# Kernel optimization log

Hardware: AMD Instinct MI355X
Metric: run time of the kernel (lower is better)

The kernel has to match this reference:

```python
import jax, jax.numpy as jnp
import numpy as np

B, S, D, H = 1, 2048, 4096, 32
HD = D // H
THETA = 10000.0
IN_SCALE = 0.1   # input_scale buffer
Q_SCALE = 0.1    # q_proj_scale buffer
K_SCALE = 0.1    # k_proj_scale buffer
V_SCALE = 0.1    # v_proj_scale buffer
OUT_SCALE = 0.1  # out_input_scale buffer


def _fake_q(x, scale, lo, hi):
    # round-to-int + clamp, kept in float (faithful to int8 fake-quant)
    return jnp.clip(jnp.round(x / scale), lo, hi)


def _w4a8_linear(x, qw, w_scale, in_scale):
    # int8 fake-quantized activation x int4-valued weight, dequant output
    qx = _fake_q(x, in_scale, -128, 127)
    return jnp.einsum('bsd,od->bso', qx, qw) * (in_scale * w_scale)


def _rope_tables(position_ids):
    inv_freq = 1.0 / (THETA ** (jnp.arange(0, HD, 2, dtype=jnp.float32) / HD))
    ang = position_ids.astype(jnp.float32)[..., None] * inv_freq  # [B,S,HD/2]
    emb = jnp.concatenate([ang, ang], axis=-1)                     # [B,S,HD]
    return jnp.cos(emb)[:, None], jnp.sin(emb)[:, None]            # [B,1,S,HD]


def _rotate_half(x):
    return jnp.concatenate([-x[..., HD // 2:], x[..., :HD // 2]], axis=-1)


def setup_inputs() -> dict:
    key = jax.random.key(0)
    ks = jax.random.split(key, 9)
    hidden_states = jax.random.normal(ks[0], (B, S, D), jnp.float32)
    def int4_w(k):
        return jnp.round(jax.random.uniform(k, (D, D), jnp.float32, -8.0, 7.0))
    def ch_scale(k):
        return jax.random.uniform(k, (D,), jnp.float32, 0.01, 0.03)
    wq, wk, wv, wo = int4_w(ks[1]), int4_w(ks[2]), int4_w(ks[3]), int4_w(ks[4])
    sq_w, sk_w, sv_w, so_w = ch_scale(ks[5]), ch_scale(ks[6]), ch_scale(ks[7]), ch_scale(ks[8])
    position_ids = jnp.arange(S, dtype=jnp.int32)[None, :]
    causal = jnp.tril(jnp.ones((S, S), dtype=bool))
    attention_mask = jnp.where(causal, 0.0, -1e9).astype(jnp.float32)[None, None]
    return dict(hidden_states=hidden_states, wq=wq, wk=wk, wv=wv, wo=wo,
                sq_w=sq_w, sk_w=sk_w, sv_w=sv_w, so_w=so_w,
                attention_mask=attention_mask, position_ids=position_ids)


def reference(hidden_states, wq, wk, wv, wo, sq_w, sk_w, sv_w, so_w,
              attention_mask, position_ids):
    # W4A8 dequant projections
    q = _w4a8_linear(hidden_states, wq, sq_w, IN_SCALE)
    k = _w4a8_linear(hidden_states, wk, sk_w, IN_SCALE)
    v = _w4a8_linear(hidden_states, wv, sv_w, IN_SCALE)
    q = q.reshape(B, S, H, HD).transpose(0, 2, 1, 3)  # [B,H,S,HD]
    k = k.reshape(B, S, H, HD).transpose(0, 2, 1, 3)
    v = v.reshape(B, S, H, HD).transpose(0, 2, 1, 3)
    # RoPE
    cos, sin = _rope_tables(position_ids)
    q = q * cos + _rotate_half(q) * sin
    k = k * cos + _rotate_half(k) * sin
    # int8 fake-quant of q/k/v, then dequant before matmuls
    q = _fake_q(q, Q_SCALE, -128, 127)
    k = _fake_q(k, K_SCALE, -128, 127)
    v = _fake_q(v, V_SCALE, -128, 127)
    scores = jnp.einsum('bhqd,bhkd->bhqk', q * Q_SCALE, k * K_SCALE) / np.sqrt(HD)
    scores = scores + attention_mask
    attn = jax.nn.softmax(scores.astype(jnp.float32), axis=-1)
    out = jnp.einsum('bhqk,bhkd->bhqd', attn, v * V_SCALE)
    out = out.transpose(0, 2, 1, 3).reshape(B, S, D)
    # o_proj input re-quantized to int8 with out_input_scale (clamp -127..127)
    out_q = _fake_q(out, OUT_SCALE, -127, 127)
    attn_output = jnp.einsum('bsd,od->bso', out_q, wo) * (OUT_SCALE * so_w)
    return attn_output
```

## Files before the change

kernel.cpp:

```cpp
#include <hip/hip_runtime.h>
#include <math.h>
#include <stdint.h>

#define S_LEN 2048
#define D_DIM 4096
#define NHEAD 32
#define HDIM  128

typedef int      v4i __attribute__((ext_vector_type(4)));
typedef float    v4f __attribute__((ext_vector_type(4)));
typedef _Float16 v8h __attribute__((ext_vector_type(8)));

__device__ __forceinline__ float quant128(float x) {
  return fminf(fmaxf(rintf(x / 0.1f), -128.f), 127.f);
}
__device__ __forceinline__ void gl_lds16(const void* g, void* l) {
  __builtin_amdgcn_global_load_lds(
      (const __attribute__((address_space(1))) void*)g,
      (__attribute__((address_space(3))) void*)l, 16, 0, 0);
}

__global__ __launch_bounds__(256) void quant_hidden_k(const float* __restrict__ in,
                                                      int8_t* __restrict__ out) {
  const int idx = blockIdx.x * 256 + threadIdx.x;
  const float4 v = ((const float4*)in)[idx];
  const int q0 = (int)quant128(v.x), q1 = (int)quant128(v.y);
  const int q2 = (int)quant128(v.z), q3 = (int)quant128(v.w);
  ((int*)out)[idx] = (q0 & 0xff) | ((q1 & 0xff) << 8) | ((q2 & 0xff) << 16) | ((q3 & 0xff) << 24);
}

__global__ __launch_bounds__(256) void wconv3_k(const float* __restrict__ a,
                                                const float* __restrict__ b,
                                                const float* __restrict__ c,
                                                int8_t* __restrict__ out) {
  const int which = blockIdx.x >> 14;
  const int sub = blockIdx.x & 16383;
  const float* src = (which == 0) ? a : (which == 1) ? b : c;
  const int idx = sub * 256 + threadIdx.x;
  const float4 v = ((const float4*)src)[idx];
  const int q0 = __float2int_rn(v.x), q1 = __float2int_rn(v.y);
  const int q2 = __float2int_rn(v.z), q3 = __float2int_rn(v.w);
  ((int*)out)[(size_t)which * 4194304 + idx] =
      (q0 & 0xff) | ((q1 & 0xff) << 8) | ((q2 & 0xff) << 16) | ((q3 & 0xff) << 24);
}

__global__ __launch_bounds__(256) void wconv_k(const float* __restrict__ in,
                                               int8_t* __restrict__ out) {
  const int idx = blockIdx.x * 256 + threadIdx.x;
  const float4 v = ((const float4*)in)[idx];
  const int q0 = __float2int_rn(v.x), q1 = __float2int_rn(v.y);
  const int q2 = __float2int_rn(v.z), q3 = __float2int_rn(v.w);
  ((int*)out)[idx] = (q0 & 0xff) | ((q1 & 0xff) << 8) | ((q2 & 0xff) << 16) | ((q3 & 0xff) << 24);
}

__global__ __launch_bounds__(256) void rope_tab_k(const int* __restrict__ pos,
                                                  float* __restrict__ ct,
                                                  float* __restrict__ st) {
  const int idx = blockIdx.x * 256 + threadIdx.x;
  const int s = idx >> 6, j = idx & 63;
  const float inv = exp2f((float)j * -0.20762050593046016f);
  const float a = (float)pos[s] * inv;
  float si, c;
  sincosf(a, &si, &c);
  ct[idx] = c;
  st[idx] = si;
}

template <int MODE>
__device__ __forceinline__ void gemm_body(
    int8_t* __restrict__ LS, const int8_t* __restrict__ A8,
    const int8_t* __restrict__ W8, const float* __restrict__ s0,
    const float* __restrict__ s1, const float* __restrict__ s2,
    const float* __restrict__ ctab, const float* __restrict__ stab,
    void* __restrict__ out0, void* __restrict__ out1, void* __restrict__ out2,
    int nwg) {
  int8_t* const Abase = LS;
  int8_t* const Bbase = LS + 49152;

  const int t = threadIdx.x;
  const int w = t >> 6, lane = t & 63, g = lane >> 4, l15 = lane & 15;
  const int wm = w >> 2, wn = w & 3;

  const int bid = blockIdx.x;
  const int lb = (bid & 7) * (nwg >> 3) + (bid >> 3);
  const int within = lb & 15, g16 = lb >> 4;
  const int bm = ((g16 & 1) * 4 + (within >> 2)) * 256;
  const int bn = ((g16 >> 1) * 4 + (within & 3)) * 256;

  const int8_t* srcA[2];
  const int8_t* srcB[2];
  int sdst[2];
#pragma unroll
  for (int i = 0; i < 2; ++i) {
    const int lin = i * 512 + t;
    const int row = lin >> 2;
    const int sc = (lin & 3) ^ ((row >> 1) & 3);
    srcA[i] = A8 + (size_t)(bm + row) * D_DIM + sc * 16;
    srcB[i] = W8 + (size_t)(bn + row) * D_DIM + sc * 16;
    sdst[i] = lin * 16;
  }

#define STAGE(KT, BI)                                                       \
  {                                                                         \
    const int kof_ = (KT) * 64;                                             \
    _Pragma("unroll") for (int i_ = 0; i_ < 2; ++i_) {                      \
      gl_lds16(srcA[i_] + kof_, Abase + (BI) * 16384 + sdst[i_]);           \
      gl_lds16(srcB[i_] + kof_, Bbase + (BI) * 16384 + sdst[i_]);           \
    }                                                                       \
  }

  const int cg = ((g ^ ((l15 >> 1) & 3)) << 4);
  const int nc0 = (wn & 1) * 32 + (wn >> 1) * 128;
  int aoffs[8], boffs[4];
#pragma unroll
  for (int mi = 0; mi < 8; ++mi)
    aoffs[mi] = (wm * 128 + mi * 16 + l15) * 64 + cg;
#pragma unroll
  for (int ni = 0; ni < 4; ++ni)
    boffs[ni] = (nc0 + (ni & 1) * 16 + (ni >> 1) * 64 + l15) * 64 + cg;

  v4i acc[8][4];
#pragma unroll
  for (int mi = 0; mi < 8; ++mi)
#pragma unroll
    for (int ni = 0; ni < 4; ++ni) acc[mi][ni] = (v4i){0, 0, 0, 0};

  STAGE(0, 0)
  STAGE(1, 1)
  asm volatile("s_waitcnt vmcnt(4)" ::: "memory");
  __builtin_amdgcn_s_barrier();
  __builtin_amdgcn_sched_barrier(0);

  for (int t3 = 0; t3 < 66; t3 += 3) {
#pragma unroll
    for (int u = 0; u < 3; ++u) {
      const int kt = t3 + u;
      if (kt < 64) {
        if (kt + 2 < 64) STAGE(kt + 2, ((u + 2) % 3))
        v4i af[8], bf[4];
        {
          const int8_t* Ab_ = Abase + u * 16384;
          const int8_t* Bb_ = Bbase + u * 16384;
#pragma unroll
          for (int mi = 0; mi < 8; ++mi) af[mi] = *(const v4i*)(Ab_ + aoffs[mi]);
#pragma unroll
          for (int ni = 0; ni < 4; ++ni) bf[ni] = *(const v4i*)(Bb_ + boffs[ni]);
        }
        __builtin_amdgcn_s_setprio(1);
#pragma unroll
        for (int mi = 0; mi < 8; ++mi)
#pragma unroll
          for (int ni = 0; ni < 4; ++ni)
            acc[mi][ni] = __builtin_amdgcn_mfma_i32_16x16x64_i8(
                af[mi], bf[ni], acc[mi][ni], 0, 0, 0);
        __builtin_amdgcn_s_setprio(0);
        if (kt + 2 < 64)
          asm volatile("s_waitcnt vmcnt(4)" ::: "memory");
        else
          asm volatile("s_waitcnt vmcnt(0)" ::: "memory");
        __builtin_amdgcn_s_barrier();
        __builtin_amdgcn_sched_barrier(0);
      }
    }
  }
#undef STAGE

  const int srow0 = bm + wm * 128;
  if (MODE == 1) {
    float* dst = (float*)out0;
#pragma unroll
    for (int ni = 0; ni < 4; ++ni) {
      const int col = bn + nc0 + (ni & 1) * 16 + (ni >> 1) * 64 + l15;
      const float sc = 0.1f * s0[col];
#pragma unroll
      for (int mi = 0; mi < 8; ++mi)
#pragma unroll
        for (int r = 0; r < 4; ++r)
          dst[(size_t)(srow0 + mi * 16 + g * 4 + r) * D_DIM + col] =
              (float)acc[mi][ni][r] * sc;
    }
  } else {
    const int seg = bn >> 12;
    const int bcol = bn & 4095;
    if (seg == 2) {
      _Float16* dst = (_Float16*)out2;
#pragma unroll
      for (int ni = 0; ni < 4; ++ni) {
        const int col = bcol + nc0 + (ni & 1) * 16 + (ni >> 1) * 64 + l15;
        const float scv = 0.1f * s2[col];
#pragma unroll
        for (int mi = 0; mi < 8; ++mi)
#pragma unroll
          for (int r = 0; r < 4; ++r) {
            const int s = srow0 + mi * 16 + g * 4 + r;
            dst[(size_t)col * S_LEN + s] = (_Float16)quant128((float)acc[mi][ni][r] * scv);
          }
      }
    } else {
      const float* wsc = seg ? s1 : s0;
      int8_t* dst = seg ? (int8_t*)out1 : (int8_t*)out0;
      const int hb = bcol + (wn >> 1) * 128;
#pragma unroll
      for (int ni = 0; ni < 2; ++ni) {
        const int dlo = (wn & 1) * 32 + ni * 16 + l15;
        const int clo = hb + dlo;
        const float sc0 = 0.1f * wsc[clo];
        const float sc1 = 0.1f * wsc[clo + 64];
#pragma unroll
        for (int mi = 0; mi < 8; ++mi)
#pragma unroll
          for (int r = 0; r < 4; ++r) {
            const int s = srow0 + mi * 16 + g * 4 + r;
            const float c = ctab[s * 64 + dlo];
            const float si = stab[s * 64 + dlo];
            const float x1 = (float)acc[mi][ni][r] * sc0;
            const float x2 = (float)acc[mi][ni + 2][r] * sc1;
            dst[(size_t)s * D_DIM + clo] = (int8_t)quant128(x1 * c - x2 * si);
            dst[(size_t)s * D_DIM + clo + 64] = (int8_t)quant128(x2 * c + x1 * si);
          }
      }
    }
  }
}

__global__ __launch_bounds__(512) void gemm_qkv(
    const int8_t* __restrict__ A8, const int8_t* __restrict__ W8,
    const float* __restrict__ s0, const float* __restrict__ s1,
    const float* __restrict__ s2, const float* __restrict__ ctab,
    const float* __restrict__ stab, void* __restrict__ out0,
    void* __restrict__ out1, void* __restrict__ out2) {
  __shared__ __align__(16) int8_t LS[6 * 16384];
  gemm_body<0>(LS, A8, W8, s0, s1, s2, ctab, stab, out0, out1, out2, 384);
}

__global__ __launch_bounds__(512) void gemm_out(
    const int8_t* __restrict__ A8, const int8_t* __restrict__ W8,
    const float* __restrict__ s0, const float* __restrict__ ctab,
    const float* __restrict__ stab, void* __restrict__ out0) {
  __shared__ __align__(16) int8_t LS[6 * 16384];
  gemm_body<1>(LS, A8, W8, s0, s0, s0, ctab, stab, out0, out0, out0, 128);
}

__global__ __launch_bounds__(512, 4) void attn_v8(
    const int8_t* __restrict__ q8, const int8_t* __restrict__ k8,
    const _Float16* __restrict__ vT, int8_t* __restrict__ o8) {
  __shared__ __align__(16) int8_t Kls[3][8192];
  __shared__ __align__(16) int8_t Vls[3][16384];
  const int jj = 15 - blockIdx.x;
  const int h = blockIdx.y;
  const int t = threadIdx.x;
  const int w = t >> 6, lane = t & 63, g = lane >> 4, l15 = lane & 15;
  const int T = 2 * jj + 2;
  const int q0 = (jj * 8 + w) * 16;
  const int q_lane = q0 + l15;
  const float SSCALE = 8.838834764831845e-4f;
  const v8h vones = {(_Float16)1, (_Float16)1, (_Float16)1, (_Float16)1,
                     (_Float16)1, (_Float16)1, (_Float16)1, (_Float16)1};

  const int ks_slot = t >> 3;
  const int ks_cs = (t & 7) ^ (ks_slot & 7);
  const int ks_key = ((ks_slot >> 5) & 1) * 32 + ((ks_slot >> 3) & 1) * 16 +
                     ((ks_slot >> 2) & 1) * 8 + ((ks_slot >> 4) & 1) * 4 +
                     (ks_slot & 3);
  const int k_src = ks_key * D_DIM + ks_cs * 16;
  const int k_dst = t * 16;
  int v_src[2], v_dst[2];
#pragma unroll
  for (int i = 0; i < 2; ++i) {
    const int lin = i * 512 + t;
    const int d = lin >> 3;
    const int cs = (lin & 7) ^ (d & 7);
    v_src[i] = d * S_LEN + cs * 8;
    v_dst[i] = lin * 16;
  }
  const int8_t* kbg = k8 + (size_t)h * HDIM;
  const _Float16* vbg = vT + (size_t)h * HDIM * S_LEN;

  auto stage = [&](int kt, int b) {
    const int8_t* ks = kbg + (size_t)kt * (64 * D_DIM);
    const _Float16* vs = vbg + kt * 64;
    gl_lds16(ks + k_src, &Kls[b][k_dst]);
#pragma unroll
    for (int i = 0; i < 2; ++i) gl_lds16(vs + v_src[i], &Vls[b][v_dst[i]]);
  };

  const v4i qa0 = *(const v4i*)(q8 + (size_t)q_lane * D_DIM + h * HDIM + g * 16);
  const v4i qa1 = *(const v4i*)(q8 + (size_t)q_lane * D_DIM + h * HDIM + 64 + g * 16);

  v4f o[8];
#pragma unroll
  for (int n = 0; n < 8; ++n) o[n] = (v4f){0.f, 0.f, 0.f, 0.f};
  v4f lacc = (v4f){0.f, 0.f, 0.f, 0.f};
  float m_i = -INFINITY;

  stage(0, 0);
  if (T > 1) stage(1, 1);

  int bi = 0;
  for (int kt = 0; kt < T; ++kt) {
    if (kt + 1 < T)
      asm volatile("s_waitcnt vmcnt(3)" ::: "memory");
    else
      asm volatile("s_waitcnt vmcnt(0)" ::: "memory");
    __builtin_amdgcn_s_barrier();
    __builtin_amdgcn_sched_barrier(0);
    if (kt + 2 < T) stage(kt + 2, bi >= 1 ? bi - 1 : bi + 2);

    const int ksw = (l15 & 7);
    float sc[4][4];
#pragma unroll
    for (int nt = 0; nt < 4; ++nt) {
      const int8_t* kr = &Kls[bi][(nt * 16 + l15) * 128];
      const v4i kb0 = *(const v4i*)(kr + ((g ^ ksw) * 16));
      const v4i kb1 = *(const v4i*)(kr + (((4 + g) ^ ksw) * 16));
      v4i c = (v4i){0, 0, 0, 0};
      c = __builtin_amdgcn_mfma_i32_16x16x64_i8(kb0, qa0, c, 0, 0, 0);
      c = __builtin_amdgcn_mfma_i32_16x16x64_i8(kb1, qa1, c, 0, 0, 0);
#pragma unroll
      for (int r = 0; r < 4; ++r) {
        float s = (float)c[r] * SSCALE;
        if (kt >= T - 2) {
          const int key = kt * 64 + ((nt >> 1) << 5) + ((g >> 1) << 4) +
                          ((g & 1) << 3) + ((nt & 1) << 2) + r;
          if (key > q_lane) s = -1.0e30f;
        }
        sc[nt][r] = s;
      }
    }
    float mx = fmaxf(fmaxf(fmaxf(sc[0][0], sc[0][1]), fmaxf(sc[0][2], sc[0][3])),
                     fmaxf(fmaxf(sc[1][0], sc[1][1]), fmaxf(sc[1][2], sc[1][3])));
    mx = fmaxf(mx, fmaxf(fmaxf(fmaxf(sc[2][0], sc[2][1]), fmaxf(sc[2][2], sc[2][3])),
                         fmaxf(fmaxf(sc[3][0], sc[3][1]), fmaxf(sc[3][2], sc[3][3]))));
    mx = fmaxf(mx, __shfl_xor(mx, 16));
    mx = fmaxf(mx, __shfl_xor(mx, 32));
    const float mnew = fmaxf(m_i, mx);
    const float alpha = __expf(m_i - mnew);
    m_i = mnew;

    float p[4][4];
#pragma unroll
    for (int nt = 0; nt < 4; ++nt)
#pragma unroll
      for (int r = 0; r < 4; ++r) p[nt][r] = __expf(sc[nt][r] - m_i);

    v8h ph0, ph1;
#pragma unroll
    for (int e = 0; e < 8; ++e) {
      ph0[e] = (_Float16)p[e >> 2][e & 3];
      ph1[e] = (_Float16)p[2 + (e >> 2)][e & 3];
    }
    float a_r[4];
#pragma unroll
    for (int r = 0; r < 4; ++r)
      a_r[r] = __shfl(alpha, (lane & 48) | (g * 4 + r));
#pragma unroll
    for (int n = 0; n < 8; ++n)
#pragma unroll
      for (int r = 0; r < 4; ++r) o[n][r] *= a_r[r];
#pragma unroll
    for (int r = 0; r < 4; ++r) lacc[r] *= a_r[r];

    __builtin_amdgcn_s_setprio(1);
    lacc = __builtin_amdgcn_mfma_f32_16x16x32_f16(ph0, vones, lacc, 0, 0, 0);
    lacc = __builtin_amdgcn_mfma_f32_16x16x32_f16(ph1, vones, lacc, 0, 0, 0);
#pragma unroll
    for (int nt = 0; nt < 8; ++nt) {
      const int8_t* vr = &Vls[bi][(nt * 16 + l15) * 128];
      const v8h v0 = *(const v8h*)(vr + ((g ^ ksw) * 16));
      const v8h v1 = *(const v8h*)(vr + (((4 + g) ^ ksw) * 16));
      o[nt] = __builtin_amdgcn_mfma_f32_16x16x32_f16(ph0, v0, o[nt], 0, 0, 0);
      o[nt] = __builtin_amdgcn_mfma_f32_16x16x32_f16(ph1, v1, o[nt], 0, 0, 0);
    }
    __builtin_amdgcn_s_setprio(0);

    bi = (bi == 2) ? 0 : bi + 1;
  }

#pragma unroll
  for (int r = 0; r < 4; ++r) {
    const float rL = 1.0f / lacc[r];
    const size_t row = (size_t)(q0 + g * 4 + r) * D_DIM + h * HDIM;
#pragma unroll
    for (int nt = 0; nt < 8; ++nt) {
      const int q = (int)fminf(fmaxf(rintf(o[nt][r] * rL), -127.f), 127.f);
      o8[row + nt * 16 + l15] = (int8_t)q;
    }
  }
}

extern "C" void kernel_launch(void* const* d_in, const int* in_sizes, int n_in,
                              void* d_out, int out_size, void* d_ws, size_t ws_size,
                              hipStream_t stream) {
  (void)in_sizes; (void)n_in; (void)out_size; (void)ws_size;
  const float* hidden = (const float*)d_in[0];
  const float* wq = (const float*)d_in[1];
  const float* wk = (const float*)d_in[2];
  const float* wv = (const float*)d_in[3];
  const float* wo = (const float*)d_in[4];
  const float* sq = (const float*)d_in[5];
  const float* sk = (const float*)d_in[6];
  const float* sv = (const float*)d_in[7];
  const float* so = (const float*)d_in[8];
  const int* pos = (const int*)d_in[10];
  float* out = (float*)d_out;

  char* ws = (char*)d_ws;
  int8_t* h8 = (int8_t*)ws;
  int8_t* q8 = (int8_t*)(ws + (8ull << 20));
  int8_t* k8 = (int8_t*)(ws + (16ull << 20));
  _Float16* vT = (_Float16*)(ws + (24ull << 20));
  int8_t* w8a = (int8_t*)(ws + (40ull << 20));
  int8_t* w8b = (int8_t*)(ws + (56ull << 20));
  int8_t* w8c = (int8_t*)(ws + (72ull << 20));
  float* ctab = (float*)(ws + (88ull << 20));
  float* stab = (float*)(ws + (88ull << 20) + (512ull << 10));
  int8_t* o8 = h8;

  hipLaunchKernelGGL(rope_tab_k, dim3(512), dim3(256), 0, stream, pos, ctab, stab);
  hipLaunchKernelGGL(quant_hidden_k, dim3(8192), dim3(256), 0, stream, hidden, h8);
  hipLaunchKernelGGL(wconv3_k, dim3(49152), dim3(256), 0, stream, wq, wk, wv, w8a);

  hipLaunchKernelGGL(gemm_qkv, dim3(384), dim3(512), 0, stream, h8, w8a,
                     sq, sk, sv, ctab, stab, (void*)q8, (void*)k8, (void*)vT);
  hipLaunchKernelGGL(wconv_k, dim3(16384), dim3(256), 0, stream, wo, w8a);
  hipLaunchKernelGGL(attn_v8, dim3(16, 32), dim3(512), 0, stream, q8, k8, vT, o8);
  hipLaunchKernelGGL(gemm_out, dim3(128), dim3(512), 0, stream, o8, w8a,
                     so, ctab, stab, (void*)out);
}
```

Before: 557.3 us.

## Halve GEMM M-tile to 128 and restructure pipeline with wait-before-stage loop

Shrinks the int8 GEMM block tile from 256x256 to 128x256, doubling the workgroup count for the QKV and output projections so more of the 256 CUs are occupied. Accumulators drop from 8x4 to 4x4 per wave, LDS shrinks to 72KB, and launch bounds ask for more resident blocks. The triple-buffer loop is rewritten to wait and barrier at the top of each iteration before issuing the next stage, instead of at the bottom. The cost is less reuse of each loaded B tile, which raises global and L2 traffic per MFMA.

```diff
diff --git a/kernel.cpp b/kernel.cpp
--- a/kernel.cpp
+++ b/kernel.cpp
@@ -75,7 +75,7 @@
     void* __restrict__ out0, void* __restrict__ out1, void* __restrict__ out2,
     int nwg) {
   int8_t* const Abase = LS;
-  int8_t* const Bbase = LS + 49152;
+  int8_t* const Bbase = LS + 24576;
 
   const int t = threadIdx.x;
   const int w = t >> 6, lane = t & 63, g = lane >> 4, l15 = lane & 15;
@@ -84,88 +84,84 @@
   const int bid = blockIdx.x;
   const int lb = (bid & 7) * (nwg >> 3) + (bid >> 3);
   const int within = lb & 15, g16 = lb >> 4;
-  const int bm = ((g16 & 1) * 4 + (within >> 2)) * 256;
-  const int bn = ((g16 >> 1) * 4 + (within & 3)) * 256;
-
-  const int8_t* srcA[2];
+  const int bm = ((g16 & 3) * 4 + (within >> 2)) * 128;
+  const int bn = ((g16 >> 2) * 4 + (within & 3)) * 256;
+
+  const int arow = t >> 2;
+  const int asc = (t & 3) ^ ((arow >> 1) & 3);
+  const int8_t* srcA = A8 + (size_t)(bm + arow) * D_DIM + asc * 16;
+  const int adst = t * 16;
   const int8_t* srcB[2];
-  int sdst[2];
+  int bdst[2];
 #pragma unroll
   for (int i = 0; i < 2; ++i) {
     const int lin = i * 512 + t;
     const int row = lin >> 2;
     const int sc = (lin & 3) ^ ((row >> 1) & 3);
-    srcA[i] = A8 + (size_t)(bm + row) * D_DIM + sc * 16;
     srcB[i] = W8 + (size_t)(bn + row) * D_DIM + sc * 16;
-    sdst[i] = lin * 16;
+    bdst[i] = lin * 16;
   }
 
 #define STAGE(KT, BI)                                                       \
   {                                                                         \
     const int kof_ = (KT) * 64;                                             \
-    _Pragma("unroll") for (int i_ = 0; i_ < 2; ++i_) {                      \
-      gl_lds16(srcA[i_] + kof_, Abase + (BI) * 16384 + sdst[i_]);           \
-      gl_lds16(srcB[i_] + kof_, Bbase + (BI) * 16384 + sdst[i_]);           \
-    }                                                                       \
+    gl_lds16(srcA + kof_, Abase + (BI) * 8192 + adst);                      \
+    _Pragma("unroll") for (int i_ = 0; i_ < 2; ++i_)                        \
+        gl_lds16(srcB[i_] + kof_, Bbase + (BI) * 16384 + bdst[i_]);         \
   }
 
   const int cg = ((g ^ ((l15 >> 1) & 3)) << 4);
   const int nc0 = (wn & 1) * 32 + (wn >> 1) * 128;
-  int aoffs[8], boffs[4];
-#pragma unroll
-  for (int mi = 0; mi < 8; ++mi)
-    aoffs[mi] = (wm * 128 + mi * 16 + l15) * 64 + cg;
+  int aoffs[4], boffs[4];
+#pragma unroll
+  for (int mi = 0; mi < 4; ++mi)
+    aoffs[mi] = (wm * 64 + mi * 16 + l15) * 64 + cg;
 #pragma unroll
   for (int ni = 0; ni < 4; ++ni)
     boffs[ni] = (nc0 + (ni & 1) * 16 + (ni >> 1) * 64 + l15) * 64 + cg;
 
-  v4i acc[8][4];
-#pragma unroll
-  for (int mi = 0; mi < 8; ++mi)
+  v4i acc[4][4];
+#pragma unroll
+  for (int mi = 0; mi < 4; ++mi)
 #pragma unroll
     for (int ni = 0; ni < 4; ++ni) acc[mi][ni] = (v4i){0, 0, 0, 0};
 
   STAGE(0, 0)
   STAGE(1, 1)
-  asm volatile("s_waitcnt vmcnt(4)" ::: "memory");
-  __builtin_amdgcn_s_barrier();
-  __builtin_amdgcn_sched_barrier(0);
-
-  for (int t3 = 0; t3 < 66; t3 += 3) {
-#pragma unroll
-    for (int u = 0; u < 3; ++u) {
-      const int kt = t3 + u;
-      if (kt < 64) {
-        if (kt + 2 < 64) STAGE(kt + 2, ((u + 2) % 3))
-        v4i af[8], bf[4];
-        {
-          const int8_t* Ab_ = Abase + u * 16384;
-          const int8_t* Bb_ = Bbase + u * 16384;
-#pragma unroll
-          for (int mi = 0; mi < 8; ++mi) af[mi] = *(const v4i*)(Ab_ + aoffs[mi]);
-#pragma unroll
-          for (int ni = 0; ni < 4; ++ni) bf[ni] = *(const v4i*)(Bb_ + boffs[ni]);
-        }
-        __builtin_amdgcn_s_setprio(1);
-#pragma unroll
-        for (int mi = 0; mi < 8; ++mi)
-#pragma unroll
-          for (int ni = 0; ni < 4; ++ni)
-            acc[mi][ni] = __builtin_amdgcn_mfma_i32_16x16x64_i8(
-                af[mi], bf[ni], acc[mi][ni], 0, 0, 0);
-        __builtin_amdgcn_s_setprio(0);
-        if (kt + 2 < 64)
-          asm volatile("s_waitcnt vmcnt(4)" ::: "memory");
-        else
-          asm volatile("s_waitcnt vmcnt(0)" ::: "memory");
-        __builtin_amdgcn_s_barrier();
-        __builtin_amdgcn_sched_barrier(0);
-      }
-    }
+
+  int bi = 0;
+  for (int kt = 0; kt < 64; ++kt) {
+    if (kt + 1 < 64)
+      asm volatile("s_waitcnt vmcnt(3)" ::: "memory");
+    else
+      asm volatile("s_waitcnt vmcnt(0)" ::: "memory");
+    __builtin_amdgcn_s_barrier();
+    __builtin_amdgcn_sched_barrier(0);
+    if (kt + 2 < 64) STAGE(kt + 2, bi >= 1 ? bi - 1 : 2)
+
+    v4i af[4], bf[4];
+    {
+      const int8_t* Ab_ = Abase + bi * 8192;
+      const int8_t* Bb_ = Bbase + bi * 16384;
+#pragma unroll
+      for (int mi = 0; mi < 4; ++mi) af[mi] = *(const v4i*)(Ab_ + aoffs[mi]);
+#pragma unroll
+      for (int ni = 0; ni < 4; ++ni) bf[ni] = *(const v4i*)(Bb_ + boffs[ni]);
+    }
+    __builtin_amdgcn_s_setprio(1);
+#pragma unroll
+    for (int mi = 0; mi < 4; ++mi)
+#pragma unroll
+      for (int ni = 0; ni < 4; ++ni)
+        acc[mi][ni] = __builtin_amdgcn_mfma_i32_16x16x64_i8(
+            af[mi], bf[ni], acc[mi][ni], 0, 0, 0);
+    __builtin_amdgcn_s_setprio(0);
+
+    bi = (bi == 2) ? 0 : bi + 1;
   }
 #undef STAGE
 
-  const int srow0 = bm + wm * 128;
+  const int srow0 = bm + wm * 64;
   if (MODE == 1) {
     float* dst = (float*)out0;
 #pragma unroll
@@ -173,7 +169,7 @@
       const int col = bn + nc0 + (ni & 1) * 16 + (ni >> 1) * 64 + l15;
       const float sc = 0.1f * s0[col];
 #pragma unroll
-      for (int mi = 0; mi < 8; ++mi)
+      for (int mi = 0; mi < 4; ++mi)
 #pragma unroll
         for (int r = 0; r < 4; ++r)
           dst[(size_t)(srow0 + mi * 16 + g * 4 + r) * D_DIM + col] =
@@ -189,7 +185,7 @@
         const int col = bcol + nc0 + (ni & 1) * 16 + (ni >> 1) * 64 + l15;
         const float scv = 0.1f * s2[col];
 #pragma unroll
-        for (int mi = 0; mi < 8; ++mi)
+        for (int mi = 0; mi < 4; ++mi)
 #pragma unroll
           for (int r = 0; r < 4; ++r) {
             const int s = srow0 + mi * 16 + g * 4 + r;
@@ -207,7 +203,7 @@
         const float sc0 = 0.1f * wsc[clo];
         const float sc1 = 0.1f * wsc[clo + 64];
 #pragma unroll
-        for (int mi = 0; mi < 8; ++mi)
+        for (int mi = 0; mi < 4; ++mi)
 #pragma unroll
           for (int r = 0; r < 4; ++r) {
             const int s = srow0 + mi * 16 + g * 4 + r;
@@ -223,22 +219,22 @@
   }
 }
 
-__global__ __launch_bounds__(512) void gemm_qkv(
+__global__ __launch_bounds__(512, 4) void gemm_qkv(
     const int8_t* __restrict__ A8, const int8_t* __restrict__ W8,
     const float* __restrict__ s0, const float* __restrict__ s1,
     const float* __restrict__ s2, const float* __restrict__ ctab,
     const float* __restrict__ stab, void* __restrict__ out0,
     void* __restrict__ out1, void* __restrict__ out2) {
-  __shared__ __align__(16) int8_t LS[6 * 16384];
-  gemm_body<0>(LS, A8, W8, s0, s1, s2, ctab, stab, out0, out1, out2, 384);
-}
-
-__global__ __launch_bounds__(512) void gemm_out(
+  __shared__ __align__(16) int8_t LS[3 * 8192 + 3 * 16384];
+  gemm_body<0>(LS, A8, W8, s0, s1, s2, ctab, stab, out0, out1, out2, 768);
+}
+
+__global__ __launch_bounds__(512, 4) void gemm_out(
     const int8_t* __restrict__ A8, const int8_t* __restrict__ W8,
     const float* __restrict__ s0, const float* __restrict__ ctab,
     const float* __restrict__ stab, void* __restrict__ out0) {
-  __shared__ __align__(16) int8_t LS[6 * 16384];
-  gemm_body<1>(LS, A8, W8, s0, s0, s0, ctab, stab, out0, out0, out0, 128);
+  __shared__ __align__(16) int8_t LS[3 * 8192 + 3 * 16384];
+  gemm_body<1>(LS, A8, W8, s0, s0, s0, ctab, stab, out0, out0, out0, 256);
 }
 
 __global__ __launch_bounds__(512, 4) void attn_v8(
@@ -420,10 +416,10 @@
   hipLaunchKernelGGL(quant_hidden_k, dim3(8192), dim3(256), 0, stream, hidden, h8);
   hipLaunchKernelGGL(wconv3_k, dim3(49152), dim3(256), 0, stream, wq, wk, wv, w8a);
 
-  hipLaunchKernelGGL(gemm_qkv, dim3(384), dim3(512), 0, stream, h8, w8a,
+  hipLaunchKernelGGL(gemm_qkv, dim3(768), dim3(512), 0, stream, h8, w8a,
                      sq, sk, sv, ctab, stab, (void*)q8, (void*)k8, (void*)vT);
   hipLaunchKernelGGL(wconv_k, dim3(16384), dim3(256), 0, stream, wo, w8a);
   hipLaunchKernelGGL(attn_v8, dim3(16, 32), dim3(512), 0, stream, q8, k8, vT, o8);
-  hipLaunchKernelGGL(gemm_out, dim3(128), dim3(512), 0, stream, o8, w8a,
+  hipLaunchKernelGGL(gemm_out, dim3(256), dim3(512), 0, stream, o8, w8a,
                      so, ctab, stab, (void*)out);
 }
```

Measured after the change: 520.8 us. 6.5% less time.

## Split int8 GEMM k-step into two half-phases interleaving LDS reads and async loads

Applied to the files above, without the earlier changes.

Restructures the main int8 MFMA loop of the projection GEMM. Each k-tile is now processed in two halves of four M-fragments, and the global-to-LDS async loads for tile kt+2 are split into per-unit issues interleaved between the halves. The 3-way unrolled loop is replaced by a rolled loop with a rotating buffer index. This halves the A-fragment registers and spreads memory traffic more evenly across MFMA bursts, at the cost of extra barriers per k-step and runtime buffer index arithmetic.

```diff
diff --git a/kernel.cpp b/kernel.cpp
--- a/kernel.cpp
+++ b/kernel.cpp
@@ -87,26 +87,25 @@
   const int bm = ((g16 & 1) * 4 + (within >> 2)) * 256;
   const int bn = ((g16 >> 1) * 4 + (within & 3)) * 256;
 
+  const int srow = t >> 2;
+  const int sc16 = ((t & 3) ^ ((srow >> 1) & 3)) * 16;
+  const int sdst = t * 16;
   const int8_t* srcA[2];
   const int8_t* srcB[2];
-  int sdst[2];
-#pragma unroll
-  for (int i = 0; i < 2; ++i) {
-    const int lin = i * 512 + t;
-    const int row = lin >> 2;
-    const int sc = (lin & 3) ^ ((row >> 1) & 3);
-    srcA[i] = A8 + (size_t)(bm + row) * D_DIM + sc * 16;
-    srcB[i] = W8 + (size_t)(bn + row) * D_DIM + sc * 16;
-    sdst[i] = lin * 16;
-  }
-
-#define STAGE(KT, BI)                                                       \
+#pragma unroll
+  for (int u = 0; u < 2; ++u) {
+    srcA[u] = A8 + (size_t)(bm + u * 128 + srow) * D_DIM + sc16;
+    srcB[u] = W8 + (size_t)(bn + u * 128 + srow) * D_DIM + sc16;
+  }
+
+#define STAGE_UNIT(KT, BUF, U)                                              \
   {                                                                         \
     const int kof_ = (KT) * 64;                                             \
-    _Pragma("unroll") for (int i_ = 0; i_ < 2; ++i_) {                      \
-      gl_lds16(srcA[i_] + kof_, Abase + (BI) * 16384 + sdst[i_]);           \
-      gl_lds16(srcB[i_] + kof_, Bbase + (BI) * 16384 + sdst[i_]);           \
-    }                                                                       \
+    if ((U) < 2)                                                            \
+      gl_lds16(srcA[(U)] + kof_, Abase + (BUF) * 16384 + (U) * 8192 + sdst);\
+    else                                                                    \
+      gl_lds16(srcB[(U) - 2] + kof_,                                        \
+               Bbase + (BUF) * 16384 + ((U) - 2) * 8192 + sdst);            \
   }
 
   const int cg = ((g ^ ((l15 >> 1) & 3)) << 4);
@@ -125,45 +124,77 @@
 #pragma unroll
     for (int ni = 0; ni < 4; ++ni) acc[mi][ni] = (v4i){0, 0, 0, 0};
 
-  STAGE(0, 0)
-  STAGE(1, 1)
+#pragma unroll
+  for (int u = 0; u < 4; ++u) STAGE_UNIT(0, 0, u)
+#pragma unroll
+  for (int u = 0; u < 4; ++u) STAGE_UNIT(1, 1, u)
   asm volatile("s_waitcnt vmcnt(4)" ::: "memory");
   __builtin_amdgcn_s_barrier();
   __builtin_amdgcn_sched_barrier(0);
 
-  for (int t3 = 0; t3 < 66; t3 += 3) {
-#pragma unroll
-    for (int u = 0; u < 3; ++u) {
-      const int kt = t3 + u;
-      if (kt < 64) {
-        if (kt + 2 < 64) STAGE(kt + 2, ((u + 2) % 3))
-        v4i af[8], bf[4];
-        {
-          const int8_t* Ab_ = Abase + u * 16384;
-          const int8_t* Bb_ = Bbase + u * 16384;
-#pragma unroll
-          for (int mi = 0; mi < 8; ++mi) af[mi] = *(const v4i*)(Ab_ + aoffs[mi]);
-#pragma unroll
-          for (int ni = 0; ni < 4; ++ni) bf[ni] = *(const v4i*)(Bb_ + boffs[ni]);
-        }
-        __builtin_amdgcn_s_setprio(1);
-#pragma unroll
-        for (int mi = 0; mi < 8; ++mi)
-#pragma unroll
-          for (int ni = 0; ni < 4; ++ni)
-            acc[mi][ni] = __builtin_amdgcn_mfma_i32_16x16x64_i8(
-                af[mi], bf[ni], acc[mi][ni], 0, 0, 0);
-        __builtin_amdgcn_s_setprio(0);
-        if (kt + 2 < 64)
-          asm volatile("s_waitcnt vmcnt(4)" ::: "memory");
-        else
-          asm volatile("s_waitcnt vmcnt(0)" ::: "memory");
-        __builtin_amdgcn_s_barrier();
-        __builtin_amdgcn_sched_barrier(0);
-      }
-    }
-  }
-#undef STAGE
+  v4i af[4], bf[4];
+  int bi = 0;
+  for (int kt = 0; kt < 64; ++kt) {
+    const int bs = (bi >= 1) ? bi - 1 : 2;
+    {
+      const int8_t* Ab_ = Abase + bi * 16384;
+      const int8_t* Bb_ = Bbase + bi * 16384;
+#pragma unroll
+      for (int ni = 0; ni < 4; ++ni) bf[ni] = *(const v4i*)(Bb_ + boffs[ni]);
+#pragma unroll
+      for (int mi = 0; mi < 4; ++mi) af[mi] = *(const v4i*)(Ab_ + aoffs[mi]);
+    }
+    if (kt + 2 < 64) {
+      STAGE_UNIT(kt + 2, bs, 0)
+      STAGE_UNIT(kt + 2, bs, 1)
+    }
+    __builtin_amdgcn_s_barrier();
+    asm volatile("s_waitcnt lgkmcnt(0)" ::: "memory");
+    __builtin_amdgcn_sched_barrier(0);
+    __builtin_amdgcn_s_setprio(1);
+#pragma unroll
+    for (int mi = 0; mi < 4; ++mi)
+#pragma unroll
+      for (int ni = 0; ni < 4; ++ni)
+        acc[mi][ni] = __builtin_amdgcn_mfma_i32_16x16x64_i8(
+            af[mi], bf[ni], acc[mi][ni], 0, 0, 0);
+    __builtin_amdgcn_s_setprio(0);
+    __builtin_amdgcn_s_barrier();
+    __builtin_amdgcn_sched_barrier(0);
+
+    {
+      const int8_t* Ab_ = Abase + bi * 16384;
+#pragma unroll
+      for (int mi = 0; mi < 4; ++mi)
+        af[mi] = *(const v4i*)(Ab_ + aoffs[4 + mi]);
+    }
+    if (kt + 2 < 64) {
+      STAGE_UNIT(kt + 2, bs, 2)
+      STAGE_UNIT(kt + 2, bs, 3)
+    }
+    __builtin_amdgcn_s_barrier();
+    asm volatile("s_waitcnt lgkmcnt(0)" ::: "memory");
+    __builtin_amdgcn_sched_barrier(0);
+    __builtin_amdgcn_s_setprio(1);
+#pragma unroll
+    for (int mi = 0; mi < 4; ++mi)
+#pragma unroll
+      for (int ni = 0; ni < 4; ++ni)
+        acc[4 + mi][ni] = __builtin_amdgcn_mfma_i32_16x16x64_i8(
+            af[mi], bf[ni], acc[4 + mi][ni], 0, 0, 0);
+    __builtin_amdgcn_s_setprio(0);
+    if (kt + 1 < 64) {
+      if (kt + 2 < 64)
+        asm volatile("s_waitcnt vmcnt(4)" ::: "memory");
+      else
+        asm volatile("s_waitcnt vmcnt(0)" ::: "memory");
+    }
+    __builtin_amdgcn_s_barrier();
+    __builtin_amdgcn_sched_barrier(0);
+
+    bi = (bi == 2) ? 0 : bi + 1;
+  }
+#undef STAGE_UNIT
 
   const int srow0 = bm + wm * 128;
   if (MODE == 1) {
```

After: 554.2 us. Within noise of the previous version (-0.6%).
